# Kernel optimization log

Hardware: AMD Instinct MI355X
Metric: run time of the kernel (lower is better)

Reference implementation:

```python
import jax, jax.numpy as jnp
import numpy as np

D_MODEL = 1024
N_HEADS = 16
D_K = D_MODEL // N_HEADS


def setup_inputs() -> dict:
    key = jax.random.key(0)
    ks = jax.random.split(key, 9)
    s = 1.0 / np.sqrt(D_MODEL)
    inp = {
        "x": jax.random.normal(ks[0], (2, 2048, D_MODEL), dtype=jnp.float32),
        "wq": jax.random.uniform(ks[1], (D_MODEL, D_MODEL), jnp.float32, -s, s),
        "bq": jax.random.uniform(ks[2], (D_MODEL,), jnp.float32, -s, s),
        "wk": jax.random.uniform(ks[3], (D_MODEL, D_MODEL), jnp.float32, -s, s),
        "bk": jax.random.uniform(ks[4], (D_MODEL,), jnp.float32, -s, s),
        "wv": jax.random.uniform(ks[5], (D_MODEL, D_MODEL), jnp.float32, -s, s),
        "bv": jax.random.uniform(ks[6], (D_MODEL,), jnp.float32, -s, s),
        "wo": jax.random.uniform(ks[7], (D_MODEL, D_MODEL), jnp.float32, -s, s),
        "bo": jax.random.uniform(ks[8], (D_MODEL,), jnp.float32, -s, s),
    }
    return inp


def reference(x, wq, bq, wk, bk, wv, bv, wo, bo):
    B, S, _ = x.shape
    # projections; weights stored as [in, out] (torch Linear applies x @ W^T; here W pre-transposed)
    def proj(w, b):
        y = x @ w + b  # [B,S,D]
        return y.reshape(B, S, N_HEADS, D_K).transpose(0, 2, 1, 3)  # [B,H,S,dk]
    q, k, v = proj(wq, bq), proj(wk, bk), proj(wv, bv)
    scores = jnp.einsum('bhqd,bhkd->bhqk', q, k) / jnp.sqrt(jnp.float32(D_K))
    attn = jax.nn.softmax(scores, axis=-1)  # dropout p=0 -> identity
    ctx = jnp.einsum('bhqk,bhkd->bhqd', attn, v)
    ctx = ctx.transpose(0, 2, 1, 3).reshape(B, S, D_MODEL)
    return ctx @ wo + bo
```

## Files before the change

kernel.cpp:

```cpp
#include <hip/hip_runtime.h>
#include <hip/hip_bf16.h>
#include <math.h>


typedef __attribute__((ext_vector_type(8))) short bf8v;
typedef __attribute__((ext_vector_type(4))) float f32x4;

constexpr int Dm = 1024;
constexpr int NH = 16;
constexpr int DK = 64;
constexpr int BB = 2;
constexpr int SS = 2048;
constexpr int MM = BB * SS;

__device__ __forceinline__ unsigned short f2bf(float f) {
  union { float f; unsigned u; } v; v.f = f;
  unsigned r = v.u + 0x7fffu + ((v.u >> 16) & 1u);
  return (unsigned short)(r >> 16);
}

__device__ __forceinline__ unsigned cvt_pk_bf16(float lo, float hi) {
  unsigned r;
  asm("v_cvt_pk_bf16_f32 %0, %1, %2" : "=v"(r) : "v"(lo), "v"(hi));
  return r;
}

__device__ __forceinline__ void gl_lds16(const void* g, void* l) {
  __builtin_amdgcn_global_load_lds(
      (const __attribute__((address_space(1))) void*)g,
      (__attribute__((address_space(3))) void*)l, 16, 0, 0);
}

__device__ __forceinline__ int swz4(int r) { return (r ^ (r >> 2)) & 3; }
__device__ __forceinline__ bf8v frag4(const unsigned short* base, int R, int s0) {
  return *(const bf8v*)((const char*)base + R * 64 + ((s0 ^ swz4(R)) << 4));
}
__device__ __forceinline__ bf8v frag8(const unsigned short* base, int R, int s0) {
  return *(const bf8v*)((const char*)base + R * 128 + (((s0 ^ R) & 7) << 4));
}

__global__ __launch_bounds__(256) void transw_kernel(
    const float* __restrict__ w0, const float* __restrict__ w1,
    const float* __restrict__ w2, const float* __restrict__ w3,
    unsigned short* __restrict__ dstBase)
{
  const float* src = (blockIdx.y == 0) ? w0 : (blockIdx.y == 1) ? w1
                   : (blockIdx.y == 2) ? w2 : w3;
  unsigned short* dst = dstBase + (size_t)blockIdx.y * (Dm * Dm);
  int idx = blockIdx.x * 256 + threadIdx.x;
  int i = idx & (Dm - 1);
  int o = (idx >> 10) << 2;
  float4 v = *(const float4*)(src + (size_t)i * Dm + o);
  dst[(size_t)(o + 0) * Dm + i] = f2bf(v.x);
  dst[(size_t)(o + 1) * Dm + i] = f2bf(v.y);
  dst[(size_t)(o + 2) * Dm + i] = f2bf(v.z);
  dst[(size_t)(o + 3) * Dm + i] = f2bf(v.w);
}

__global__ __launch_bounds__(256) void proj_kernel(
    const float* __restrict__ x, const unsigned short* __restrict__ WtBase,
    const float* __restrict__ bq, const float* __restrict__ bk, const float* __restrict__ bv,
    unsigned short* __restrict__ Qh, unsigned short* __restrict__ Kh,
    unsigned short* __restrict__ Vh)
{
  __shared__ unsigned short As[2][128 * 32];
  __shared__ unsigned short Bs[2][128 * 32];
  const int z = blockIdx.z;
  const unsigned short* W = WtBase + (size_t)z * (Dm * Dm);
  const float* bias = (z == 0) ? bq : (z == 1) ? bk : bv;

  const int tid = threadIdx.x, lane = tid & 63, wave = tid >> 6;
  const int wm = wave >> 1, wn = wave & 1;
  const int m0 = blockIdx.y * 128, n0 = blockIdx.x * 128;
  const int l15 = lane & 15, l4 = lane >> 4;

  const int q1 = tid, q2 = tid + 256;
  const int rw1 = q1 >> 2, sl1 = q1 & 3, c1 = sl1 ^ swz4(rw1);
  const int rw2 = q2 >> 2, sl2 = q2 & 3, c2 = sl2 ^ swz4(rw2);
  const int ldsOff1 = (q1 - lane) * 16, ldsOff2 = (q2 - lane) * 16;

  f32x4 acc[4][4] = {};
  float4 a1, a1b, a2, a2b;

  auto loadA = [&](int k0) {
    const float* s1 = x + (size_t)(m0 + rw1) * Dm + k0 + c1 * 8;
    const float* s2 = x + (size_t)(m0 + rw2) * Dm + k0 + c2 * 8;
    a1 = *(const float4*)s1; a1b = *(const float4*)(s1 + 4);
    a2 = *(const float4*)s2; a2b = *(const float4*)(s2 + 4);
  };
  auto stageB = [&](int buf, int k0) {
    gl_lds16(W + (size_t)(n0 + rw1) * Dm + k0 + c1 * 8, (char*)Bs[buf] + ldsOff1);
    gl_lds16(W + (size_t)(n0 + rw2) * Dm + k0 + c2 * 8, (char*)Bs[buf] + ldsOff2);
  };
  auto writeA = [&](int buf) {
    bf8v v;
    v[0] = (short)f2bf(a1.x);  v[1] = (short)f2bf(a1.y);
    v[2] = (short)f2bf(a1.z);  v[3] = (short)f2bf(a1.w);
    v[4] = (short)f2bf(a1b.x); v[5] = (short)f2bf(a1b.y);
    v[6] = (short)f2bf(a1b.z); v[7] = (short)f2bf(a1b.w);
    *(bf8v*)((char*)As[buf] + rw1 * 64 + (sl1 << 4)) = v;
    v[0] = (short)f2bf(a2.x);  v[1] = (short)f2bf(a2.y);
    v[2] = (short)f2bf(a2.z);  v[3] = (short)f2bf(a2.w);
    v[4] = (short)f2bf(a2b.x); v[5] = (short)f2bf(a2b.y);
    v[6] = (short)f2bf(a2b.z); v[7] = (short)f2bf(a2b.w);
    *(bf8v*)((char*)As[buf] + rw2 * 64 + (sl2 << 4)) = v;
  };

  loadA(0);
  stageB(0, 0);
  writeA(0);
  __syncthreads();

  for (int k0 = 0; k0 < Dm; k0 += 32) {
    const int cur = (k0 >> 5) & 1, nxt = cur ^ 1;
    const bool more = (k0 + 32) < Dm;
    if (more) { loadA(k0 + 32); stageB(nxt, k0 + 32); }

    bf8v af[4], bfr[4];
    #pragma unroll
    for (int i = 0; i < 4; ++i) af[i] = frag4(As[cur], wm * 64 + i * 16 + l15, l4);
    #pragma unroll
    for (int j = 0; j < 4; ++j) bfr[j] = frag4(Bs[cur], wn * 64 + j * 16 + l15, l4);
    __builtin_amdgcn_s_setprio(1);
    #pragma unroll
    for (int i = 0; i < 4; ++i)
      #pragma unroll
      for (int j = 0; j < 4; ++j)
        acc[i][j] = __builtin_amdgcn_mfma_f32_16x16x32_bf16(af[i], bfr[j], acc[i][j], 0, 0, 0);
    __builtin_amdgcn_s_setprio(0);

    if (more) writeA(nxt);
    __syncthreads();
  }

  unsigned short* Out = (z == 0) ? Qh : (z == 1) ? Kh : Vh;
  const float oscale = (z == 0) ? 0.18033688011112042f : 1.0f;
  #pragma unroll
  for (int i = 0; i < 4; ++i)
    #pragma unroll
    for (int j = 0; j < 4; ++j) {
      int row = m0 + wm * 64 + i * 16 + l4 * 4;
      int col = n0 + wn * 64 + j * 16 + l15;
      float bcol = bias[col];
      int h = col >> 6, d = col & 63;
      #pragma unroll
      for (int r = 0; r < 4; ++r) {
        int rr = row + r;
        int b = rr >> 11, s = rr & 2047;
        unsigned short val = f2bf((acc[i][j][r] + bcol) * oscale);
        if (z < 2)
          Out[(((size_t)(b * NH + h) * SS + s) * DK) + d] = val;
        else
          Out[((size_t)(b * NH + h) * DK + d) * SS + s] = val;
      }
    }
}

__global__ __launch_bounds__(256) void outproj_kernel(
    const unsigned short* __restrict__ Ctx, const unsigned short* __restrict__ Wto,
    const float* __restrict__ bo, float* __restrict__ Out)
{
  __shared__ unsigned short As[2][128 * 32];
  __shared__ unsigned short Bs[2][128 * 32];
  const int tid = threadIdx.x, lane = tid & 63, wave = tid >> 6;
  const int wm = wave >> 1, wn = wave & 1;
  const int m0 = blockIdx.y * 128, n0 = blockIdx.x * 128;
  const int l15 = lane & 15, l4 = lane >> 4;

  const int q1 = tid, q2 = tid + 256;
  const int rw1 = q1 >> 2, sl1 = q1 & 3, c1 = sl1 ^ swz4(rw1);
  const int rw2 = q2 >> 2, sl2 = q2 & 3, c2 = sl2 ^ swz4(rw2);
  const int ldsOff1 = (q1 - lane) * 16, ldsOff2 = (q2 - lane) * 16;

  auto srcA = [&](int rw, int c, int k0) -> const unsigned short* {
    int rr = m0 + rw, b = rr >> 11, s = rr & 2047;
    int col = k0 + c * 8, h = col >> 6, d = col & 63;
    return Ctx + ((size_t)(b * NH + h) * SS + s) * DK + d;
  };
  auto stageAB = [&](int buf, int k0) {
    gl_lds16(srcA(rw1, c1, k0), (char*)As[buf] + ldsOff1);
    gl_lds16(srcA(rw2, c2, k0), (char*)As[buf] + ldsOff2);
    gl_lds16(Wto + (size_t)(n0 + rw1) * Dm + k0 + c1 * 8, (char*)Bs[buf] + ldsOff1);
    gl_lds16(Wto + (size_t)(n0 + rw2) * Dm + k0 + c2 * 8, (char*)Bs[buf] + ldsOff2);
  };

  f32x4 acc[4][4] = {};

  stageAB(0, 0);
  __syncthreads();

  for (int k0 = 0; k0 < Dm; k0 += 32) {
    const int cur = (k0 >> 5) & 1, nxt = cur ^ 1;
    if (k0 + 32 < Dm) stageAB(nxt, k0 + 32);

    bf8v af[4], bfr[4];
    #pragma unroll
    for (int i = 0; i < 4; ++i) af[i] = frag4(As[cur], wm * 64 + i * 16 + l15, l4);
    #pragma unroll
    for (int j = 0; j < 4; ++j) bfr[j] = frag4(Bs[cur], wn * 64 + j * 16 + l15, l4);
    __builtin_amdgcn_s_setprio(1);
    #pragma unroll
    for (int i = 0; i < 4; ++i)
      #pragma unroll
      for (int j = 0; j < 4; ++j)
        acc[i][j] = __builtin_amdgcn_mfma_f32_16x16x32_bf16(af[i], bfr[j], acc[i][j], 0, 0, 0);
    __builtin_amdgcn_s_setprio(0);
    __syncthreads();
  }

  #pragma unroll
  for (int i = 0; i < 4; ++i)
    #pragma unroll
    for (int j = 0; j < 4; ++j) {
      int row = m0 + wm * 64 + i * 16 + l4 * 4;
      int col = n0 + wn * 64 + j * 16 + l15;
      float bcol = bo[col];
      #pragma unroll
      for (int r = 0; r < 4; ++r)
        Out[(size_t)(row + r) * Dm + col] = acc[i][j][r] + bcol;
    }
}

constexpr int PSTR = 88;

__global__ __launch_bounds__(256) void attn_kernel(
    const unsigned short* __restrict__ Q, const unsigned short* __restrict__ K,
    const unsigned short* __restrict__ Vt, unsigned short* __restrict__ CtxQ)
{
  __shared__ unsigned short Kl[2][64 * 64];
  __shared__ unsigned short Vl[2][64 * 64];
  __shared__ unsigned short Pt[4][32 * PSTR];

  const int tid = threadIdx.x, lane = tid & 63, wave = tid >> 6;
  const int l15 = lane & 15, g = lane >> 4;
  const int bh = blockIdx.y;
  const int q0 = blockIdx.x * 128 + wave * 32;
  const size_t base = (size_t)bh * SS * DK;

  bf8v qf[2][2];
  #pragma unroll
  for (int i = 0; i < 2; ++i)
    #pragma unroll
    for (int kk = 0; kk < 2; ++kk)
      qf[i][kk] = *(const bf8v*)(Q + base + (size_t)(q0 + i * 16 + l15) * DK + kk * 32 + g * 8);

  float m = -INFINITY;
  float lpart[2] = {0.f, 0.f};
  f32x4 cacc[2][4] = {};

  auto stage = [&](int bsel, int kt) {
    #pragma unroll
    for (int it = 0; it < 2; ++it) {
      int q = tid + 256 * it;
      int row = q >> 3, sl = q & 7, c = sl ^ (row & 7);
      gl_lds16(K + base + (size_t)(kt + row) * DK + c * 8,
               (char*)Kl[bsel] + (size_t)(q - lane) * 16);
      gl_lds16(Vt + base + (size_t)row * SS + kt + c * 8,
               (char*)Vl[bsel] + (size_t)(q - lane) * 16);
    }
  };

  constexpr int NT = SS / 64;
  stage(0, 0);
  __syncthreads();
  int cur = 0;

  for (int t = 0; t < NT; ++t) {
    if (t + 1 < NT) stage(cur ^ 1, (t + 1) * 64);
    const unsigned short* Kb = Kl[cur];
    const unsigned short* Vb = Vl[cur];

    f32x4 st[2][4] = {};
    __builtin_amdgcn_s_setprio(1);
    #pragma unroll
    for (int j = 0; j < 4; ++j)
      #pragma unroll
      for (int kk = 0; kk < 2; ++kk) {
        bf8v kf = frag8(Kb, j * 16 + l15, kk * 4 + g);
        st[0][j] = __builtin_amdgcn_mfma_f32_16x16x32_bf16(kf, qf[0][kk], st[0][j], 0, 0, 0);
        st[1][j] = __builtin_amdgcn_mfma_f32_16x16x32_bf16(kf, qf[1][kk], st[1][j], 0, 0, 0);
      }
    __builtin_amdgcn_s_setprio(0);

    float mx = st[0][0][0];
    #pragma unroll
    for (int i = 0; i < 2; ++i)
      #pragma unroll
      for (int j = 0; j < 4; ++j)
        #pragma unroll
        for (int r = 0; r < 4; ++r) mx = fmaxf(mx, st[i][j][r]);
    mx = fmaxf(mx, __shfl_xor(mx, 1));
    mx = fmaxf(mx, __shfl_xor(mx, 2));
    mx = fmaxf(mx, __shfl_xor(mx, 4));
    mx = fmaxf(mx, __shfl_xor(mx, 8));
    mx = fmaxf(mx, __shfl_xor(mx, 16));
    mx = fmaxf(mx, __shfl_xor(mx, 32));

    if (mx - m > 8.0f) {
      float mnew = mx;
      float alpha = exp2f(m - mnew);
      m = mnew;
      lpart[0] *= alpha; lpart[1] *= alpha;
      #pragma unroll
      for (int i = 0; i < 2; ++i)
        #pragma unroll
        for (int n = 0; n < 4; ++n)
          #pragma unroll
          for (int r = 0; r < 4; ++r) cacc[i][n][r] *= alpha;
    }

    #pragma unroll
    for (int i = 0; i < 2; ++i) {
      unsigned short* prow = &Pt[wave][(i * 16 + l15) * PSTR];
      #pragma unroll
      for (int j = 0; j < 4; ++j) {
        float p0 = exp2f(st[i][j][0] - m);
        float p1 = exp2f(st[i][j][1] - m);
        float p2 = exp2f(st[i][j][2] - m);
        float p3 = exp2f(st[i][j][3] - m);
        lpart[i] += (p0 + p1) + (p2 + p3);
        *(unsigned*)(prow + j * 16 + 4 * g)     = cvt_pk_bf16(p0, p1);
        *(unsigned*)(prow + j * 16 + 4 * g + 2) = cvt_pk_bf16(p2, p3);
      }
    }

    __builtin_amdgcn_s_setprio(1);
    #pragma unroll
    for (int kk = 0; kk < 2; ++kk) {
      bf8v pb[2];
      #pragma unroll
      for (int i = 0; i < 2; ++i)
        pb[i] = *(const bf8v*)&Pt[wave][(i * 16 + l15) * PSTR + kk * 32 + 8 * g];
      #pragma unroll
      for (int n = 0; n < 4; ++n) {
        bf8v vb = frag8(Vb, n * 16 + l15, kk * 4 + g);
        cacc[0][n] = __builtin_amdgcn_mfma_f32_16x16x32_bf16(vb, pb[0], cacc[0][n], 0, 0, 0);
        cacc[1][n] = __builtin_amdgcn_mfma_f32_16x16x32_bf16(vb, pb[1], cacc[1][n], 0, 0, 0);
      }
    }
    __builtin_amdgcn_s_setprio(0);

    __syncthreads();
    cur ^= 1;
  }

  #pragma unroll
  for (int i = 0; i < 2; ++i) {
    float lf = lpart[i];
    lf += __shfl_xor(lf, 16);
    lf += __shfl_xor(lf, 32);
    float inv = 1.0f / lf;
    int s = q0 + i * 16 + l15;
    #pragma unroll
    for (int n = 0; n < 4; ++n) {
      uint2 w;
      w.x = cvt_pk_bf16(cacc[i][n][0] * inv, cacc[i][n][1] * inv);
      w.y = cvt_pk_bf16(cacc[i][n][2] * inv, cacc[i][n][3] * inv);
      *(uint2*)(CtxQ + base + (size_t)s * DK + n * 16 + g * 4) = w;
    }
  }
}

extern "C" void kernel_launch(void* const* d_in, const int* in_sizes, int n_in,
                              void* d_out, int out_size, void* d_ws, size_t ws_size,
                              hipStream_t stream) {
  const float* x  = (const float*)d_in[0];
  const float* wq = (const float*)d_in[1];
  const float* bq = (const float*)d_in[2];
  const float* wk = (const float*)d_in[3];
  const float* bk = (const float*)d_in[4];
  const float* wv = (const float*)d_in[5];
  const float* bv = (const float*)d_in[6];
  const float* wo = (const float*)d_in[7];
  const float* bo = (const float*)d_in[8];
  float* out = (float*)d_out;

  unsigned short* ws = (unsigned short*)d_ws;
  const size_t WPLANE = (size_t)Dm * Dm;
  const size_t PLANE  = (size_t)MM * Dm;
  unsigned short* Wt  = ws;
  unsigned short* Qh  = ws + PLANE;
  unsigned short* Kh  = ws + 2 * PLANE;
  unsigned short* Vh  = ws + 3 * PLANE;
  unsigned short* Wto = Wt + 3 * WPLANE;

  dim3 blk(256);
  transw_kernel<<<dim3(1024, 4), blk, 0, stream>>>(wq, wk, wv, wo, Wt);
  proj_kernel<<<dim3(Dm / 128, MM / 128, 3), blk, 0, stream>>>(
      x, Wt, bq, bk, bv, Qh, Kh, Vh);
  attn_kernel<<<dim3(SS / 128, BB * NH), blk, 0, stream>>>(Qh, Kh, Vh, Qh);
  outproj_kernel<<<dim3(Dm / 128, MM / 128), blk, 0, stream>>>(Qh, Wto, bo, out);
}
```

Measured before the change: 157.9 us.

## Rewrite attention with 32x32 MFMA, in-register P, and split-KV across waves

The attention kernel moves from 16x16x32 to 32x32x16 bf16 MFMA. The softmax probabilities are repacked in registers with v_permlane32_swap instead of round-tripping through an LDS P buffer. Blocks grow to 512 threads, and two wave groups each handle half of the key sequence, with the partial results merged through shared memory at the end. This is meant to cut LDS traffic and the number of MFMA issues and to add parallelism per query tile. The cost is a final cross-wave reduction and higher register pressure under launch_bounds(512,4).

```diff
diff --git a/kernel.cpp b/kernel.cpp
--- a/kernel.cpp
+++ b/kernel.cpp
@@ -5,6 +5,9 @@
 
 typedef __attribute__((ext_vector_type(8))) short bf8v;
 typedef __attribute__((ext_vector_type(4))) float f32x4;
+typedef __attribute__((ext_vector_type(16))) float f32x16;
+
+#define mfma32(a, b, c) __builtin_amdgcn_mfma_f32_32x32x16_bf16((a), (b), (c), 0, 0, 0)
 
 constexpr int Dm = 1024;
 constexpr int NH = 16;
@@ -25,6 +28,10 @@
   return r;
 }
 
+__device__ __forceinline__ void swap32(unsigned &a, unsigned &b) {
+  asm("v_permlane32_swap_b32 %0, %1" : "+v"(a), "+v"(b));
+}
+
 __device__ __forceinline__ void gl_lds16(const void* g, void* l) {
   __builtin_amdgcn_global_load_lds(
       (const __attribute__((address_space(1))) void*)g,
@@ -35,8 +42,8 @@
 __device__ __forceinline__ bf8v frag4(const unsigned short* base, int R, int s0) {
   return *(const bf8v*)((const char*)base + R * 64 + ((s0 ^ swz4(R)) << 4));
 }
-__device__ __forceinline__ bf8v frag8(const unsigned short* base, int R, int s0) {
-  return *(const bf8v*)((const char*)base + R * 128 + (((s0 ^ R) & 7) << 4));
+__device__ __forceinline__ bf8v rd8(const unsigned short* base, int row, int slot) {
+  return *(const bf8v*)((const char*)base + row * 128 + (((slot ^ row) & 7) << 4));
 }
 
 __global__ __launch_bounds__(256) void transw_kernel(
@@ -221,74 +228,64 @@
     }
 }
 
-constexpr int PSTR = 88;
-
-__global__ __launch_bounds__(256) void attn_kernel(
+__global__ __launch_bounds__(512, 4) void attn_kernel(
     const unsigned short* __restrict__ Q, const unsigned short* __restrict__ K,
     const unsigned short* __restrict__ Vt, unsigned short* __restrict__ CtxQ)
 {
-  __shared__ unsigned short Kl[2][64 * 64];
-  __shared__ unsigned short Vl[2][64 * 64];
-  __shared__ unsigned short Pt[4][32 * PSTR];
+  __shared__ __align__(16) unsigned short smem[32768];
+  unsigned short* KlB = smem;
+  unsigned short* VlB = smem + 16384;
 
   const int tid = threadIdx.x, lane = tid & 63, wave = tid >> 6;
-  const int l15 = lane & 15, g = lane >> 4;
+  const int qsub = wave & 3, khalf = wave >> 2;
+  const int l31 = lane & 31, hi = lane >> 5;
   const int bh = blockIdx.y;
-  const int q0 = blockIdx.x * 128 + wave * 32;
+  const int q0 = blockIdx.x * 128 + qsub * 32;
   const size_t base = (size_t)bh * SS * DK;
 
-  bf8v qf[2][2];
+  bf8v qf[4];
   #pragma unroll
-  for (int i = 0; i < 2; ++i)
-    #pragma unroll
-    for (int kk = 0; kk < 2; ++kk)
-      qf[i][kk] = *(const bf8v*)(Q + base + (size_t)(q0 + i * 16 + l15) * DK + kk * 32 + g * 8);
-
-  float m = -INFINITY;
-  float lpart[2] = {0.f, 0.f};
-  f32x4 cacc[2][4] = {};
-
-  auto stage = [&](int bsel, int kt) {
-    #pragma unroll
-    for (int it = 0; it < 2; ++it) {
-      int q = tid + 256 * it;
-      int row = q >> 3, sl = q & 7, c = sl ^ (row & 7);
-      gl_lds16(K + base + (size_t)(kt + row) * DK + c * 8,
-               (char*)Kl[bsel] + (size_t)(q - lane) * 16);
-      gl_lds16(Vt + base + (size_t)row * SS + kt + c * 8,
-               (char*)Vl[bsel] + (size_t)(q - lane) * 16);
-    }
-  };
-
-  constexpr int NT = SS / 64;
+  for (int dc = 0; dc < 4; ++dc)
+    qf[dc] = *(const bf8v*)(Q + base + (size_t)(q0 + l31) * DK + dc * 16 + hi * 8);
+
+  float m = -INFINITY, lpart = 0.f;
+  f32x16 cacc[2] = {};
+
+  const int srow = tid >> 3, ssl = tid & 7, sc = ssl ^ (srow & 7);
+  const int soff = (tid - lane) * 16;
+  auto kslab = [&](int buf, int h) { return KlB + (buf * 2 + h) * 4096; };
+  auto vslab = [&](int buf, int h) { return VlB + (buf * 2 + h) * 4096; };
+  auto stage = [&](int buf, int kt) {
+    gl_lds16(K + base + (size_t)(kt + srow) * DK + sc * 8,          (char*)kslab(buf, 0) + soff);
+    gl_lds16(K + base + (size_t)(1024 + kt + srow) * DK + sc * 8,   (char*)kslab(buf, 1) + soff);
+    gl_lds16(Vt + base + (size_t)srow * SS + kt + sc * 8,           (char*)vslab(buf, 0) + soff);
+    gl_lds16(Vt + base + (size_t)srow * SS + 1024 + kt + sc * 8,    (char*)vslab(buf, 1) + soff);
+  };
+
+  constexpr int NT = 16;
   stage(0, 0);
   __syncthreads();
-  int cur = 0;
 
   for (int t = 0; t < NT; ++t) {
+    const int cur = t & 1;
     if (t + 1 < NT) stage(cur ^ 1, (t + 1) * 64);
-    const unsigned short* Kb = Kl[cur];
-    const unsigned short* Vb = Vl[cur];
-
-    f32x4 st[2][4] = {};
+    const unsigned short* Kb = kslab(cur, khalf);
+    const unsigned short* Vb = vslab(cur, khalf);
+
+    f32x16 st0 = {}, st1 = {};
     __builtin_amdgcn_s_setprio(1);
     #pragma unroll
-    for (int j = 0; j < 4; ++j)
-      #pragma unroll
-      for (int kk = 0; kk < 2; ++kk) {
-        bf8v kf = frag8(Kb, j * 16 + l15, kk * 4 + g);
-        st[0][j] = __builtin_amdgcn_mfma_f32_16x16x32_bf16(kf, qf[0][kk], st[0][j], 0, 0, 0);
-        st[1][j] = __builtin_amdgcn_mfma_f32_16x16x32_bf16(kf, qf[1][kk], st[1][j], 0, 0, 0);
-      }
+    for (int dc = 0; dc < 4; ++dc) {
+      bf8v kf0 = rd8(Kb, l31, dc * 2 + hi);
+      bf8v kf1 = rd8(Kb, 32 + l31, dc * 2 + hi);
+      st0 = mfma32(kf0, qf[dc], st0);
+      st1 = mfma32(kf1, qf[dc], st1);
+    }
     __builtin_amdgcn_s_setprio(0);
 
-    float mx = st[0][0][0];
-    #pragma unroll
-    for (int i = 0; i < 2; ++i)
-      #pragma unroll
-      for (int j = 0; j < 4; ++j)
-        #pragma unroll
-        for (int r = 0; r < 4; ++r) mx = fmaxf(mx, st[i][j][r]);
+    float mx = -INFINITY;
+    #pragma unroll
+    for (int r = 0; r < 16; ++r) mx = fmaxf(mx, fmaxf(st0[r], st1[r]));
     mx = fmaxf(mx, __shfl_xor(mx, 1));
     mx = fmaxf(mx, __shfl_xor(mx, 2));
     mx = fmaxf(mx, __shfl_xor(mx, 4));
@@ -297,67 +294,82 @@
     mx = fmaxf(mx, __shfl_xor(mx, 32));
 
     if (mx - m > 8.0f) {
-      float mnew = mx;
-      float alpha = exp2f(m - mnew);
-      m = mnew;
-      lpart[0] *= alpha; lpart[1] *= alpha;
-      #pragma unroll
-      for (int i = 0; i < 2; ++i)
+      float alpha = exp2f(m - mx);
+      m = mx;
+      lpart *= alpha;
+      #pragma unroll
+      for (int n = 0; n < 2; ++n)
         #pragma unroll
-        for (int n = 0; n < 4; ++n)
-          #pragma unroll
-          for (int r = 0; r < 4; ++r) cacc[i][n][r] *= alpha;
+        for (int r = 0; r < 16; ++r) cacc[n][r] *= alpha;
     }
 
-    #pragma unroll
-    for (int i = 0; i < 2; ++i) {
-      unsigned short* prow = &Pt[wave][(i * 16 + l15) * PSTR];
+    auto process = [&](const f32x16& st, int ktile) {
+      float p[16];
+      #pragma unroll
+      for (int r = 0; r < 16; ++r) p[r] = exp2f(st[r] - m);
+      float sA = ((p[0] + p[1]) + (p[2] + p[3])) + ((p[4] + p[5]) + (p[6] + p[7]));
+      float sB = ((p[8] + p[9]) + (p[10] + p[11])) + ((p[12] + p[13]) + (p[14] + p[15]));
+      lpart += sA + sB;
+      #pragma unroll
+      for (int c = 0; c < 2; ++c) {
+        const int o = c * 8;
+        unsigned A  = cvt_pk_bf16(p[o + 0], p[o + 1]);
+        unsigned B  = cvt_pk_bf16(p[o + 4], p[o + 5]);
+        unsigned Cw = cvt_pk_bf16(p[o + 2], p[o + 3]);
+        unsigned Dw = cvt_pk_bf16(p[o + 6], p[o + 7]);
+        swap32(A, B); swap32(Cw, Dw);
+        union { bf8v v; unsigned w[4]; } pf;
+        pf.w[0] = A; pf.w[1] = Cw; pf.w[2] = B; pf.w[3] = Dw;
+        const int slot = ktile * 4 + c * 2 + hi;
+        bf8v vb0 = rd8(Vb, l31, slot);
+        bf8v vb1 = rd8(Vb, 32 + l31, slot);
+        __builtin_amdgcn_s_setprio(1);
+        cacc[0] = mfma32(vb0, pf.v, cacc[0]);
+        cacc[1] = mfma32(vb1, pf.v, cacc[1]);
+        __builtin_amdgcn_s_setprio(0);
+      }
+    };
+    process(st0, 0);
+    process(st1, 1);
+
+    __syncthreads();
+  }
+
+  float lf = lpart + __shfl_xor(lpart, 32);
+  float* scr = (float*)smem;
+  float* fs = scr + qsub * 2176;
+
+  if (khalf == 1) {
+    #pragma unroll
+    for (int n = 0; n < 2; ++n)
+      #pragma unroll
+      for (int r = 0; r < 16; ++r)
+        fs[(n * 16 + r) * 64 + lane] = cacc[n][r];
+    fs[2048 + lane] = lf;
+    if (lane == 0) fs[2048 + 64] = m;
+  }
+  __syncthreads();
+  if (khalf == 0) {
+    float mB = fs[2048 + 64];
+    float lB = fs[2048 + lane];
+    float mt = fmaxf(m, mB);
+    float a  = exp2f(m - mt), b2 = exp2f(mB - mt);
+    float inv = 1.0f / (lf * a + lB * b2);
+    float fa = a * inv, fb = b2 * inv;
+    #pragma unroll
+    for (int n = 0; n < 2; ++n)
       #pragma unroll
       for (int j = 0; j < 4; ++j) {
-        float p0 = exp2f(st[i][j][0] - m);
-        float p1 = exp2f(st[i][j][1] - m);
-        float p2 = exp2f(st[i][j][2] - m);
-        float p3 = exp2f(st[i][j][3] - m);
-        lpart[i] += (p0 + p1) + (p2 + p3);
-        *(unsigned*)(prow + j * 16 + 4 * g)     = cvt_pk_bf16(p0, p1);
-        *(unsigned*)(prow + j * 16 + 4 * g + 2) = cvt_pk_bf16(p2, p3);
+        float v0 = cacc[n][4 * j + 0] * fa + fs[(n * 16 + 4 * j + 0) * 64 + lane] * fb;
+        float v1 = cacc[n][4 * j + 1] * fa + fs[(n * 16 + 4 * j + 1) * 64 + lane] * fb;
+        float v2 = cacc[n][4 * j + 2] * fa + fs[(n * 16 + 4 * j + 2) * 64 + lane] * fb;
+        float v3 = cacc[n][4 * j + 3] * fa + fs[(n * 16 + 4 * j + 3) * 64 + lane] * fb;
+        uint2 w;
+        w.x = cvt_pk_bf16(v0, v1);
+        w.y = cvt_pk_bf16(v2, v3);
+        int d = n * 32 + 8 * j + 4 * hi;
+        *(uint2*)(CtxQ + base + (size_t)(q0 + l31) * DK + d) = w;
       }
-    }
-
-    __builtin_amdgcn_s_setprio(1);
-    #pragma unroll
-    for (int kk = 0; kk < 2; ++kk) {
-      bf8v pb[2];
-      #pragma unroll
-      for (int i = 0; i < 2; ++i)
-        pb[i] = *(const bf8v*)&Pt[wave][(i * 16 + l15) * PSTR + kk * 32 + 8 * g];
-      #pragma unroll
-      for (int n = 0; n < 4; ++n) {
-        bf8v vb = frag8(Vb, n * 16 + l15, kk * 4 + g);
-        cacc[0][n] = __builtin_amdgcn_mfma_f32_16x16x32_bf16(vb, pb[0], cacc[0][n], 0, 0, 0);
-        cacc[1][n] = __builtin_amdgcn_mfma_f32_16x16x32_bf16(vb, pb[1], cacc[1][n], 0, 0, 0);
-      }
-    }
-    __builtin_amdgcn_s_setprio(0);
-
-    __syncthreads();
-    cur ^= 1;
-  }
-
-  #pragma unroll
-  for (int i = 0; i < 2; ++i) {
-    float lf = lpart[i];
-    lf += __shfl_xor(lf, 16);
-    lf += __shfl_xor(lf, 32);
-    float inv = 1.0f / lf;
-    int s = q0 + i * 16 + l15;
-    #pragma unroll
-    for (int n = 0; n < 4; ++n) {
-      uint2 w;
-      w.x = cvt_pk_bf16(cacc[i][n][0] * inv, cacc[i][n][1] * inv);
-      w.y = cvt_pk_bf16(cacc[i][n][2] * inv, cacc[i][n][3] * inv);
-      *(uint2*)(CtxQ + base + (size_t)s * DK + n * 16 + g * 4) = w;
-    }
   }
 }
 
@@ -384,10 +396,9 @@
   unsigned short* Vh  = ws + 3 * PLANE;
   unsigned short* Wto = Wt + 3 * WPLANE;
 
-  dim3 blk(256);
-  transw_kernel<<<dim3(1024, 4), blk, 0, stream>>>(wq, wk, wv, wo, Wt);
-  proj_kernel<<<dim3(Dm / 128, MM / 128, 3), blk, 0, stream>>>(
+  transw_kernel<<<dim3(1024, 4), dim3(256), 0, stream>>>(wq, wk, wv, wo, Wt);
+  proj_kernel<<<dim3(Dm / 128, MM / 128, 3), dim3(256), 0, stream>>>(
       x, Wt, bq, bk, bv, Qh, Kh, Vh);
-  attn_kernel<<<dim3(SS / 128, BB * NH), blk, 0, stream>>>(Qh, Kh, Vh, Qh);
-  outproj_kernel<<<dim3(Dm / 128, MM / 128), blk, 0, stream>>>(Qh, Wto, bo, out);
-}
+  attn_kernel<<<dim3(SS / 128, BB * NH), dim3(512), 0, stream>>>(Qh, Kh, Vh, Qh);
+  outproj_kernel<<<dim3(Dm / 128, MM / 128), dim3(256), 0, stream>>>(Qh, Wto, bo, out);
+}
```

Result: faster. 151.2 us (-4.3%).
